# Kernel optimization log

Measured on AMD Instinct MI355X. Metric: run time of the kernel, lower is better.

## Reference

```python
import jax, jax.numpy as jnp
import numpy as np

B, S, D, H = 8, 1024, 1024, 16
HD = D // H  # head_dim = 64
SCALE = HD ** -0.5


def setup_inputs() -> dict:
    key = jax.random.key(0)
    ks = jax.random.split(key, 10)
    std = D ** -0.5
    return {
        "hidden_states": jax.random.normal(ks[0], (B, S, D), jnp.float32),
        "attn_mask": jnp.zeros((B, 1, S, S), jnp.float32),
        "prev_attn_weights": jax.random.normal(ks[1], (B, H, S, S), jnp.float32),
        "Wq": jax.random.normal(ks[2], (D, D), jnp.float32) * std,
        "bq": jnp.zeros((D,), jnp.float32),
        "Wk": jax.random.normal(ks[3], (D, D), jnp.float32) * std,
        "bk": jnp.zeros((D,), jnp.float32),
        "Wv": jax.random.normal(ks[4], (D, D), jnp.float32) * std,
        "bv": jnp.zeros((D,), jnp.float32),
    }


def _split_heads(x):
    # (B, S, D) -> (B, H, S, HD)
    return x.reshape(B, S, H, HD).transpose(0, 2, 1, 3)


def reference(hidden_states, attn_mask, prev_attn_weights, Wq, bq, Wk, bk, Wv, bv):
    q = _split_heads(hidden_states @ Wq + bq)
    k = _split_heads(hidden_states @ Wk + bk)
    v = _split_heads(hidden_states @ Wv + bv)
    # scaled dot-product scores + additive mask + realformer residual scores
    scores = jnp.einsum("bhqd,bhkd->bhqk", q, k) * SCALE
    scores = scores + attn_mask + prev_attn_weights
    probs = jax.nn.softmax(scores, axis=-1)  # dropout p=0 (eval)
    ctx = jnp.einsum("bhqk,bhkd->bhqd", probs, v)
    # (B, H, S, HD) -> (B, S, D)
    out = ctx.transpose(0, 2, 1, 3).reshape(B, S, D)
    return out
```

## Files before the change

### kernel.cpp

```cpp
#include <hip/hip_runtime.h>

#define B_  8
#define S_  1024
#define D_  1024
#define H_  16
#define HD_ 64
#define M_  8192
#define LOG2E 1.44269504088896f
#define QSCALE_ (0.125f * 1.44269504088896f)
#define MSHIFT_ 20.0f

typedef __attribute__((ext_vector_type(8))) short bf16x8;
typedef __attribute__((ext_vector_type(4))) float f32x4;

__device__ __forceinline__ unsigned short f2b(float x) {
  union { float f; unsigned u; } un; un.f = x;
  unsigned r = un.u + 0x7FFFu + ((un.u >> 16) & 1u);
  return (unsigned short)(r >> 16);
}

__global__ __launch_bounds__(256) void k_convert_x(const float* __restrict__ x,
                                                   unsigned short* __restrict__ o) {
  int i = (blockIdx.x * 256 + threadIdx.x) * 4;
  const int n = M_ * D_;
  const int stride = gridDim.x * 256 * 4;
  for (; i < n; i += stride) {
    const float4 v = *(const float4*)(x + i);
    ushort4 r;
    r.x = f2b(v.x); r.y = f2b(v.y); r.z = f2b(v.z); r.w = f2b(v.w);
    *(ushort4*)(o + i) = r;
  }
}

__global__ __launch_bounds__(256) void k_transpose_w(const float* __restrict__ Wq,
    const float* __restrict__ Wk, const float* __restrict__ Wv,
    unsigned short* __restrict__ Wt) {
  __shared__ float t[64][65];
  const float* W = (blockIdx.z == 0) ? Wq : ((blockIdx.z == 1) ? Wk : Wv);
  unsigned short* dst = Wt + (size_t)blockIdx.z * (D_ * D_);
  const int k0 = blockIdx.x * 64, n0 = blockIdx.y * 64;
  const int tid = threadIdx.x;
#pragma unroll
  for (int i = 0; i < 16; ++i) {
    const int lin = i * 256 + tid;
    const int r = lin >> 6, c = lin & 63;
    t[r][c] = W[(size_t)(k0 + r) * D_ + n0 + c];
  }
  __syncthreads();
#pragma unroll
  for (int i = 0; i < 16; ++i) {
    const int lin = i * 256 + tid;
    const int r = lin >> 6, c = lin & 63;
    dst[(size_t)(n0 + r) * D_ + k0 + c] = f2b(t[c][r]);
  }
}

template <int MODE>
__global__ __launch_bounds__(256) void k_proj(const unsigned short* __restrict__ X,
    const unsigned short* __restrict__ Wt,
    const float* __restrict__ bq, const float* __restrict__ bk, const float* __restrict__ bv,
    unsigned short* __restrict__ Qw, unsigned short* __restrict__ Kw,
    unsigned short* __restrict__ Vt) {
  __shared__ unsigned short xs[128 * 32];
  __shared__ unsigned short wsh[128 * 32];
  const int tid = threadIdx.x;
  const int lane = tid & 63, wv = tid >> 6;
  const int g = lane >> 4, li = lane & 15;
  const int m0 = blockIdx.x * 128;
  const int n0 = blockIdx.y * 128;
  const int wr = wv >> 1, wc = wv & 1;
  const int wtrow0 = (MODE == 0) ? n0 : (2048 + n0);

  f32x4 acc[4][4];
#pragma unroll
  for (int i = 0; i < 4; ++i)
#pragma unroll
    for (int j = 0; j < 4; ++j) acc[i][j] = (f32x4){0.f, 0.f, 0.f, 0.f};

  const int srow = wv * 32 + (lane >> 2);
  const int skel = (lane & 3) * 8;

  for (int k0 = 0; k0 < D_; k0 += 32) {
#pragma unroll
    for (int i = 0; i < 2; ++i) {
      const unsigned short* gx = X + (size_t)(m0 + srow + i * 16) * D_ + k0 + skel;
      const unsigned short* gw = Wt + (size_t)(wtrow0 + srow + i * 16) * D_ + k0 + skel;
      __builtin_amdgcn_global_load_lds(
          (const __attribute__((address_space(1))) void*)gx,
          (__attribute__((address_space(3))) void*)&xs[(wv * 32 + i * 16) * 32], 16, 0, 0);
      __builtin_amdgcn_global_load_lds(
          (const __attribute__((address_space(1))) void*)gw,
          (__attribute__((address_space(3))) void*)&wsh[(wv * 32 + i * 16) * 32], 16, 0, 0);
    }
    __syncthreads();
    bf16x8 af[4], bfr[4];
#pragma unroll
    for (int i = 0; i < 4; ++i) {
      const int ar = wr * 64 + i * 16 + li;
      const int br = wc * 64 + i * 16 + li;
      if (MODE == 0) {
        af[i]  = *(const bf16x8*)&xs[ar * 32 + g * 8];
        bfr[i] = *(const bf16x8*)&wsh[br * 32 + g * 8];
      } else {
        af[i]  = *(const bf16x8*)&wsh[ar * 32 + g * 8];
        bfr[i] = *(const bf16x8*)&xs[br * 32 + g * 8];
      }
    }
#pragma unroll
    for (int i = 0; i < 4; ++i)
#pragma unroll
      for (int j = 0; j < 4; ++j)
        acc[i][j] = __builtin_amdgcn_mfma_f32_16x16x32_bf16(af[i], bfr[j], acc[i][j], 0, 0, 0);
    __syncthreads();
  }

  if (MODE == 0) {
#pragma unroll
    for (int j = 0; j < 4; ++j) {
      const int n = n0 + wc * 64 + j * 16 + li;
      const float bias = (n < D_) ? bq[n] : bk[n - D_];
#pragma unroll
      for (int i = 0; i < 4; ++i) {
#pragma unroll
        for (int r = 0; r < 4; ++r) {
          const int m = m0 + wr * 64 + i * 16 + g * 4 + r;
          const float v = acc[i][j][r] + bias;
          const int bb = m >> 10, ss = m & 1023;
          if (n < D_) {
            Qw[((size_t)(bb * H_ + (n >> 6)) * S_ + ss) * HD_ + (n & 63)] = f2b(v * QSCALE_);
          } else {
            const int nk = n - D_;
            Kw[((size_t)(bb * H_ + (nk >> 6)) * S_ + ss) * HD_ + (nk & 63)] = f2b(v);
          }
        }
      }
    }
  } else {
#pragma unroll
    for (int i = 0; i < 4; ++i) {
#pragma unroll
      for (int r = 0; r < 4; ++r) {
        const int nv = n0 + wr * 64 + i * 16 + g * 4 + r;
        const float bias = bv[nv];
#pragma unroll
        for (int j = 0; j < 4; ++j) {
          const int m = m0 + wc * 64 + j * 16 + li;
          const int bb = m >> 10, ss = m & 1023;
          const float v = acc[i][j][r] + bias;
          Vt[((size_t)(bb * H_ + (nv >> 6)) * HD_ + (nv & 63)) * S_ + ss] = f2b(v);
        }
      }
    }
  }
}

__global__ __launch_bounds__(256, 2) void k_attn(const unsigned short* __restrict__ Qw,
    const unsigned short* __restrict__ Kw, const unsigned short* __restrict__ Vt,
    const float* __restrict__ prev, const float* __restrict__ mask,
    float* __restrict__ out) {
  __shared__ unsigned short k_s[2][4096];
  __shared__ unsigned short v_s[2][4096];
  __shared__ float pm_s[2][4][4][64][4];
  __shared__ unsigned short p_lds[4][16][72];
  const int tid = threadIdx.x;
  const int lane = tid & 63, wv = tid >> 6;
  const int g = lane >> 4, li = lane & 15;

  const int phys = blockIdx.x + 16 * blockIdx.y;
  const int xcd = phys & 7, idx = phys >> 3;
  const int qt = idx & 15;
  const int bh = xcd + 8 * (idx >> 4);
  const int b = bh >> 4, h = bh & 15;
  const int q0 = qt * 64 + wv * 16;

  const float* pdma = prev + (size_t)bh * S_ * S_ + (size_t)(q0 + li) * S_ + g * 4;
  const float* mb   = mask + (size_t)b * S_ * S_ + (size_t)(q0 + li) * S_ + g * 4;
  const unsigned short* kbase = Kw + (size_t)bh * S_ * HD_;
  const unsigned short* vbase = Vt + (size_t)bh * HD_ * S_;

  bf16x8 qf[2];
  {
    const unsigned short* qp = Qw + ((size_t)bh * S_ + q0 + li) * HD_ + g * 8;
    qf[0] = *(const bf16x8*)qp;
    qf[1] = *(const bf16x8*)(qp + 32);
  }

  const int dr0 = (0 * 256 + tid) >> 3, dc0 = (0 * 256 + tid) & 7;
  const int dr1 = (1 * 256 + tid) >> 3, dc1 = (1 * 256 + tid) & 7;
  const int sc0 = ((dc0 ^ (dr0 & 7)) << 3);
  const int sc1 = ((dc1 ^ (dr1 & 7)) << 3);

#define STAGE(TN, BI)                                                                      \
  {                                                                                        \
    const int sn = (TN) * 64;                                                              \
    __builtin_amdgcn_global_load_lds(                                                      \
        (const __attribute__((address_space(1))) void*)(kbase + (size_t)(sn + dr0) * HD_ + sc0), \
        (__attribute__((address_space(3))) void*)(&k_s[BI][0] + wv * 512), 16, 0, 0);      \
    __builtin_amdgcn_global_load_lds(                                                      \
        (const __attribute__((address_space(1))) void*)(kbase + (size_t)(sn + dr1) * HD_ + sc1), \
        (__attribute__((address_space(3))) void*)(&k_s[BI][0] + 2048 + wv * 512), 16, 0, 0); \
    __builtin_amdgcn_global_load_lds(                                                      \
        (const __attribute__((address_space(1))) void*)(vbase + (size_t)dr0 * S_ + sn + sc0), \
        (__attribute__((address_space(3))) void*)(&v_s[BI][0] + wv * 512), 16, 0, 0);      \
    __builtin_amdgcn_global_load_lds(                                                      \
        (const __attribute__((address_space(1))) void*)(vbase + (size_t)dr1 * S_ + sn + sc1), \
        (__attribute__((address_space(3))) void*)(&v_s[BI][0] + 2048 + wv * 512), 16, 0, 0); \
    _Pragma("unroll")                                                                      \
    for (int cb = 0; cb < 4; ++cb)                                                         \
      __builtin_amdgcn_global_load_lds(                                                    \
          (const __attribute__((address_space(1))) void*)(pdma + sn + cb * 16),            \
          (__attribute__((address_space(3))) void*)&pm_s[BI][wv][cb][0][0], 16, 0, 0);     \
  }

  float lrun = 0.f;
  f32x4 ctx[4];
#pragma unroll
  for (int d = 0; d < 4; ++d) ctx[d] = (f32x4){0.f, 0.f, 0.f, 0.f};

  f32x4 mA[4], mB[4];

  STAGE(0, 0);
#pragma unroll
  for (int cb = 0; cb < 4; ++cb) mA[cb] = *(const f32x4*)(mb + cb * 16);

#define PHASE(T, PB, NB, MCUR, MNXT)                                                  \
  {                                                                                   \
    const int tn = ((T) < 15) ? (T) + 1 : 15;                                         \
    STAGE(tn, NB);                                                                    \
    _Pragma("unroll")                                                                 \
    for (int cb = 0; cb < 4; ++cb)                                                    \
      MNXT[cb] = *(const f32x4*)(mb + tn * 64 + cb * 16);                             \
    asm volatile("s_waitcnt vmcnt(12)" ::: "memory");                                 \
    __builtin_amdgcn_s_barrier();                                                     \
    {                                                                                 \
      const unsigned short* kb = &k_s[PB][0];                                         \
      const unsigned short* vb = &v_s[PB][0];                                         \
      f32x4 sa[4];                                                                    \
      _Pragma("unroll")                                                               \
      for (int cb = 0; cb < 4; ++cb) {                                                \
        const int r = cb * 16 + li;                                                   \
        const bf16x8 k0 = *(const bf16x8*)(kb + r * 64 + ((g ^ (li & 7)) << 3));      \
        const bf16x8 k1 = *(const bf16x8*)(kb + r * 64 + (((g + 4) ^ (li & 7)) << 3)); \
        f32x4 z = (f32x4){0.f, 0.f, 0.f, 0.f};                                        \
        z      = __builtin_amdgcn_mfma_f32_16x16x32_bf16(k0, qf[0], z, 0, 0, 0);      \
        sa[cb] = __builtin_amdgcn_mfma_f32_16x16x32_bf16(k1, qf[1], z, 0, 0, 0);      \
      }                                                                               \
      _Pragma("unroll")                                                               \
      for (int cb = 0; cb < 4; ++cb) {                                                \
        const f32x4 pv = *(const f32x4*)&pm_s[PB][wv][cb][lane][0];                   \
        f32x4 pmc;                                                                    \
        pmc.x = fmaf(pv.x + MCUR[cb].x, LOG2E, -MSHIFT_);                             \
        pmc.y = fmaf(pv.y + MCUR[cb].y, LOG2E, -MSHIFT_);                             \
        pmc.z = fmaf(pv.z + MCUR[cb].z, LOG2E, -MSHIFT_);                             \
        pmc.w = fmaf(pv.w + MCUR[cb].w, LOG2E, -MSHIFT_);                             \
        const float e0 = exp2f(sa[cb][0] + pmc.x);                                    \
        const float e1 = exp2f(sa[cb][1] + pmc.y);                                    \
        const float e2 = exp2f(sa[cb][2] + pmc.z);                                    \
        const float e3 = exp2f(sa[cb][3] + pmc.w);                                    \
        lrun += (e0 + e1) + (e2 + e3);                                                \
        ushort4 pw;                                                                   \
        pw.x = f2b(e0); pw.y = f2b(e1); pw.z = f2b(e2); pw.w = f2b(e3);               \
        *(ushort4*)&p_lds[wv][li][cb * 16 + g * 4] = pw;                              \
      }                                                                               \
      bf16x8 pf0 = *(const bf16x8*)&p_lds[wv][li][g * 8];                             \
      bf16x8 pf1 = *(const bf16x8*)&p_lds[wv][li][32 + g * 8];                        \
      _Pragma("unroll")                                                               \
      for (int d = 0; d < 4; ++d) {                                                   \
        const int r = d * 16 + li;                                                    \
        const bf16x8 v0 = *(const bf16x8*)(vb + r * 64 + ((g ^ (li & 7)) << 3));      \
        const bf16x8 v1 = *(const bf16x8*)(vb + r * 64 + (((g + 4) ^ (li & 7)) << 3)); \
        ctx[d] = __builtin_amdgcn_mfma_f32_16x16x32_bf16(pf0, v0, ctx[d], 0, 0, 0);   \
        ctx[d] = __builtin_amdgcn_mfma_f32_16x16x32_bf16(pf1, v1, ctx[d], 0, 0, 0);   \
      }                                                                               \
    }                                                                                 \
    __builtin_amdgcn_s_barrier();                                                     \
  }

  for (int t = 0; t < 16; t += 2) {
    PHASE(t,     0, 1, mA, mB);
    PHASE(t + 1, 1, 0, mB, mA);
  }
#undef PHASE
#undef STAGE

  lrun += __shfl_xor(lrun, 16);
  lrun += __shfl_xor(lrun, 32);
#pragma unroll
  for (int j = 0; j < 4; ++j) {
    const float rs = __shfl(lrun, g * 4 + j);
    const float inv = 1.0f / rs;
    const int q = q0 + g * 4 + j;
    float* op = out + ((size_t)b * S_ + q) * D_ + h * HD_ + li;
#pragma unroll
    for (int d = 0; d < 4; ++d)
      op[d * 16] = ctx[d][j] * inv;
  }
}

extern "C" void kernel_launch(void* const* d_in, const int* in_sizes, int n_in,
                              void* d_out, int out_size, void* d_ws, size_t ws_size,
                              hipStream_t stream) {
  const float* hs   = (const float*)d_in[0];
  const float* mask = (const float*)d_in[1];
  const float* prev = (const float*)d_in[2];
  const float* Wq   = (const float*)d_in[3];
  const float* bq   = (const float*)d_in[4];
  const float* Wk   = (const float*)d_in[5];
  const float* bk   = (const float*)d_in[6];
  const float* Wv   = (const float*)d_in[7];
  const float* bv   = (const float*)d_in[8];
  float* out = (float*)d_out;

  char* ws = (char*)d_ws;
  unsigned short* Xbf = (unsigned short*)ws;
  unsigned short* Wt  = (unsigned short*)(ws + (16ull << 20));
  unsigned short* Qw  = (unsigned short*)(ws + (22ull << 20));
  unsigned short* Kw  = (unsigned short*)(ws + (38ull << 20));
  unsigned short* Vt  = (unsigned short*)(ws + (54ull << 20));

  k_convert_x<<<2048, 256, 0, stream>>>(hs, Xbf);
  k_transpose_w<<<dim3(16, 16, 3), 256, 0, stream>>>(Wq, Wk, Wv, Wt);
  k_proj<0><<<dim3(64, 16), 256, 0, stream>>>(Xbf, Wt, bq, bk, bv, Qw, Kw, Vt);
  k_proj<1><<<dim3(64, 8),  256, 0, stream>>>(Xbf, Wt, bq, bk, bv, Qw, Kw, Vt);
  k_attn<<<dim3(16, 128), 256, 0, stream>>>(Qw, Kw, Vt, prev, mask, out);
}
```

Measured before the change: 285.0 us.

## Triple-buffer attention with 32-key tiles, DMA mask to LDS, add setprio

Restructures the attention main loop from a double-buffered 64-key tile into a triple-buffered 32-key tile pipeline that prefetches two tiles ahead. The additive mask is now loaded asynchronously into LDS alongside prev_attn_weights instead of through register loads. MFMA sections are wrapped with s_setprio, and the V tile layout drops the XOR swizzle. The goal is to hide the memory latency of the large prev/mask streams better, at the cost of twice as many barriers and possible LDS bank conflicts on the unswizzled V reads.

Result: slower. 311.3 us (+9.2%).

```diff
diff --git a/kernel.cpp b/kernel.cpp
--- a/kernel.cpp
+++ b/kernel.cpp
@@ -158,10 +158,11 @@
     const unsigned short* __restrict__ Kw, const unsigned short* __restrict__ Vt,
     const float* __restrict__ prev, const float* __restrict__ mask,
     float* __restrict__ out) {
-  __shared__ unsigned short k_s[2][4096];
-  __shared__ unsigned short v_s[2][4096];
-  __shared__ float pm_s[2][4][4][64][4];
-  __shared__ unsigned short p_lds[4][16][72];
+  __shared__ unsigned short k_s[3][2048];
+  __shared__ unsigned short v_s[3][2048];
+  __shared__ float pm_s[3][4][2][64][4];
+  __shared__ float mk_s[3][4][2][64][4];
+  __shared__ unsigned short p_lds[4][16][40];
   const int tid = threadIdx.x;
   const int lane = tid & 63, wv = tid >> 6;
   const int g = lane >> 4, li = lane & 15;
@@ -174,7 +175,7 @@
   const int q0 = qt * 64 + wv * 16;
 
   const float* pdma = prev + (size_t)bh * S_ * S_ + (size_t)(q0 + li) * S_ + g * 4;
-  const float* mb   = mask + (size_t)b * S_ * S_ + (size_t)(q0 + li) * S_ + g * 4;
+  const float* mdma = mask + (size_t)b * S_ * S_ + (size_t)(q0 + li) * S_ + g * 4;
   const unsigned short* kbase = Kw + (size_t)bh * S_ * HD_;
   const unsigned short* vbase = Vt + (size_t)bh * HD_ * S_;
 
@@ -185,31 +186,32 @@
     qf[1] = *(const bf16x8*)(qp + 32);
   }
 
-  const int dr0 = (0 * 256 + tid) >> 3, dc0 = (0 * 256 + tid) & 7;
-  const int dr1 = (1 * 256 + tid) >> 3, dc1 = (1 * 256 + tid) & 7;
-  const int sc0 = ((dc0 ^ (dr0 & 7)) << 3);
-  const int sc1 = ((dc1 ^ (dr1 & 7)) << 3);
+  const int krow = tid >> 3;
+  const int kcol = (((tid & 7) ^ (krow & 7)) << 3);
+  const int vrow = tid >> 2;
+  const int vcol = ((tid & 3) << 3);
 
 #define STAGE(TN, BI)                                                                      \
   {                                                                                        \
-    const int sn = (TN) * 64;                                                              \
-    __builtin_amdgcn_global_load_lds(                                                      \
-        (const __attribute__((address_space(1))) void*)(kbase + (size_t)(sn + dr0) * HD_ + sc0), \
+    const int sn = (TN) * 32;                                                              \
+    __builtin_amdgcn_global_load_lds(                                                      \
+        (const __attribute__((address_space(1))) void*)(kbase + (size_t)(sn + krow) * HD_ + kcol), \
         (__attribute__((address_space(3))) void*)(&k_s[BI][0] + wv * 512), 16, 0, 0);      \
     __builtin_amdgcn_global_load_lds(                                                      \
-        (const __attribute__((address_space(1))) void*)(kbase + (size_t)(sn + dr1) * HD_ + sc1), \
-        (__attribute__((address_space(3))) void*)(&k_s[BI][0] + 2048 + wv * 512), 16, 0, 0); \
-    __builtin_amdgcn_global_load_lds(                                                      \
-        (const __attribute__((address_space(1))) void*)(vbase + (size_t)dr0 * S_ + sn + sc0), \
+        (const __attribute__((address_space(1))) void*)(vbase + (size_t)vrow * S_ + sn + vcol), \
         (__attribute__((address_space(3))) void*)(&v_s[BI][0] + wv * 512), 16, 0, 0);      \
     __builtin_amdgcn_global_load_lds(                                                      \
-        (const __attribute__((address_space(1))) void*)(vbase + (size_t)dr1 * S_ + sn + sc1), \
-        (__attribute__((address_space(3))) void*)(&v_s[BI][0] + 2048 + wv * 512), 16, 0, 0); \
-    _Pragma("unroll")                                                                      \
-    for (int cb = 0; cb < 4; ++cb)                                                         \
-      __builtin_amdgcn_global_load_lds(                                                    \
-          (const __attribute__((address_space(1))) void*)(pdma + sn + cb * 16),            \
-          (__attribute__((address_space(3))) void*)&pm_s[BI][wv][cb][0][0], 16, 0, 0);     \
+        (const __attribute__((address_space(1))) void*)(pdma + sn),                        \
+        (__attribute__((address_space(3))) void*)&pm_s[BI][wv][0][0][0], 16, 0, 0);        \
+    __builtin_amdgcn_global_load_lds(                                                      \
+        (const __attribute__((address_space(1))) void*)(pdma + sn + 16),                   \
+        (__attribute__((address_space(3))) void*)&pm_s[BI][wv][1][0][0], 16, 0, 0);        \
+    __builtin_amdgcn_global_load_lds(                                                      \
+        (const __attribute__((address_space(1))) void*)(mdma + sn),                        \
+        (__attribute__((address_space(3))) void*)&mk_s[BI][wv][0][0][0], 16, 0, 0);        \
+    __builtin_amdgcn_global_load_lds(                                                      \
+        (const __attribute__((address_space(1))) void*)(mdma + sn + 16),                   \
+        (__attribute__((address_space(3))) void*)&mk_s[BI][wv][1][0][0], 16, 0, 0);        \
   }
 
   float lrun = 0.f;
@@ -217,42 +219,38 @@
 #pragma unroll
   for (int d = 0; d < 4; ++d) ctx[d] = (f32x4){0.f, 0.f, 0.f, 0.f};
 
-  f32x4 mA[4], mB[4];
-
   STAGE(0, 0);
-#pragma unroll
-  for (int cb = 0; cb < 4; ++cb) mA[cb] = *(const f32x4*)(mb + cb * 16);
-
-#define PHASE(T, PB, NB, MCUR, MNXT)                                                  \
+  STAGE(1, 1);
+
+#define PHASE(T, PB, NB, DOSTAGE, VM)                                                 \
   {                                                                                   \
-    const int tn = ((T) < 15) ? (T) + 1 : 15;                                         \
-    STAGE(tn, NB);                                                                    \
-    _Pragma("unroll")                                                                 \
-    for (int cb = 0; cb < 4; ++cb)                                                    \
-      MNXT[cb] = *(const f32x4*)(mb + tn * 64 + cb * 16);                             \
-    asm volatile("s_waitcnt vmcnt(12)" ::: "memory");                                 \
+    if (DOSTAGE) STAGE((T) + 2, NB);                                                  \
+    asm volatile("s_waitcnt vmcnt(" #VM ")" ::: "memory");                            \
     __builtin_amdgcn_s_barrier();                                                     \
     {                                                                                 \
       const unsigned short* kb = &k_s[PB][0];                                         \
       const unsigned short* vb = &v_s[PB][0];                                         \
-      f32x4 sa[4];                                                                    \
+      f32x4 sa[2];                                                                    \
+      __builtin_amdgcn_s_setprio(1);                                                  \
       _Pragma("unroll")                                                               \
-      for (int cb = 0; cb < 4; ++cb) {                                                \
+      for (int cb = 0; cb < 2; ++cb) {                                                \
         const int r = cb * 16 + li;                                                   \
-        const bf16x8 k0 = *(const bf16x8*)(kb + r * 64 + ((g ^ (li & 7)) << 3));      \
-        const bf16x8 k1 = *(const bf16x8*)(kb + r * 64 + (((g + 4) ^ (li & 7)) << 3)); \
+        const bf16x8 k0 = *(const bf16x8*)(kb + r * 64 + ((g ^ (r & 7)) << 3));       \
+        const bf16x8 k1 = *(const bf16x8*)(kb + r * 64 + (((g + 4) ^ (r & 7)) << 3)); \
         f32x4 z = (f32x4){0.f, 0.f, 0.f, 0.f};                                        \
         z      = __builtin_amdgcn_mfma_f32_16x16x32_bf16(k0, qf[0], z, 0, 0, 0);      \
         sa[cb] = __builtin_amdgcn_mfma_f32_16x16x32_bf16(k1, qf[1], z, 0, 0, 0);      \
       }                                                                               \
+      __builtin_amdgcn_s_setprio(0);                                                  \
       _Pragma("unroll")                                                               \
-      for (int cb = 0; cb < 4; ++cb) {                                                \
+      for (int cb = 0; cb < 2; ++cb) {                                                \
         const f32x4 pv = *(const f32x4*)&pm_s[PB][wv][cb][lane][0];                   \
+        const f32x4 mv = *(const f32x4*)&mk_s[PB][wv][cb][lane][0];                   \
         f32x4 pmc;                                                                    \
-        pmc.x = fmaf(pv.x + MCUR[cb].x, LOG2E, -MSHIFT_);                             \
-        pmc.y = fmaf(pv.y + MCUR[cb].y, LOG2E, -MSHIFT_);                             \
-        pmc.z = fmaf(pv.z + MCUR[cb].z, LOG2E, -MSHIFT_);                             \
-        pmc.w = fmaf(pv.w + MCUR[cb].w, LOG2E, -MSHIFT_);                             \
+        pmc.x = fmaf(pv.x + mv.x, LOG2E, -MSHIFT_);                                   \
+        pmc.y = fmaf(pv.y + mv.y, LOG2E, -MSHIFT_);                                   \
+        pmc.z = fmaf(pv.z + mv.z, LOG2E, -MSHIFT_);                                   \
+        pmc.w = fmaf(pv.w + mv.w, LOG2E, -MSHIFT_);                                   \
         const float e0 = exp2f(sa[cb][0] + pmc.x);                                    \
         const float e1 = exp2f(sa[cb][1] + pmc.y);                                    \
         const float e2 = exp2f(sa[cb][2] + pmc.z);                                    \
@@ -262,24 +260,25 @@
         pw.x = f2b(e0); pw.y = f2b(e1); pw.z = f2b(e2); pw.w = f2b(e3);               \
         *(ushort4*)&p_lds[wv][li][cb * 16 + g * 4] = pw;                              \
       }                                                                               \
-      bf16x8 pf0 = *(const bf16x8*)&p_lds[wv][li][g * 8];                             \
-      bf16x8 pf1 = *(const bf16x8*)&p_lds[wv][li][32 + g * 8];                        \
+      const bf16x8 pf0 = *(const bf16x8*)&p_lds[wv][li][g * 8];                       \
+      __builtin_amdgcn_s_setprio(1);                                                  \
       _Pragma("unroll")                                                               \
       for (int d = 0; d < 4; ++d) {                                                   \
-        const int r = d * 16 + li;                                                    \
-        const bf16x8 v0 = *(const bf16x8*)(vb + r * 64 + ((g ^ (li & 7)) << 3));      \
-        const bf16x8 v1 = *(const bf16x8*)(vb + r * 64 + (((g + 4) ^ (li & 7)) << 3)); \
+        const bf16x8 v0 = *(const bf16x8*)(vb + (d * 16 + li) * 32 + g * 8);          \
         ctx[d] = __builtin_amdgcn_mfma_f32_16x16x32_bf16(pf0, v0, ctx[d], 0, 0, 0);   \
-        ctx[d] = __builtin_amdgcn_mfma_f32_16x16x32_bf16(pf1, v1, ctx[d], 0, 0, 0);   \
       }                                                                               \
+      __builtin_amdgcn_s_setprio(0);                                                  \
     }                                                                                 \
     __builtin_amdgcn_s_barrier();                                                     \
   }
 
-  for (int t = 0; t < 16; t += 2) {
-    PHASE(t,     0, 1, mA, mB);
-    PHASE(t + 1, 1, 0, mB, mA);
-  }
+  for (int t = 0; t < 30; t += 3) {
+    PHASE(t,     0, 2, 1, 12);
+    PHASE(t + 1, 1, 0, 1, 12);
+    PHASE(t + 2, 2, 1, 1, 12);
+  }
+  PHASE(30, 0, 2, 0, 6);
+  PHASE(31, 1, 0, 0, 0);
 #undef PHASE
 #undef STAGE
 
```

## Coalesce prev-score DMA with swizzled rows, merge projection launches

Applied to the files above, without the earlier changes.

The prev_attn_weights tile is now loaded as full 256-byte row segments per wave, with an XOR swizzle in LDS, instead of 16-byte pieces spread across many rows. K/V staging is reorganised so each wave loads its own rows. The two templated projection kernels are merged into one launch that picks its mode from blockIdx.y, which removes a launch and lets the Q/K and V work share the GPU. The merged kernel branches on mode at runtime instead of at compile time, and a final vmcnt wait is added after the attention loop.

Result: faster. 267.8 us (-6.0%).

```diff
diff --git a/kernel.cpp b/kernel.cpp
--- a/kernel.cpp
+++ b/kernel.cpp
@@ -55,7 +55,6 @@
   }
 }
 
-template <int MODE>
 __global__ __launch_bounds__(256) void k_proj(const unsigned short* __restrict__ X,
     const unsigned short* __restrict__ Wt,
     const float* __restrict__ bq, const float* __restrict__ bk, const float* __restrict__ bv,
@@ -67,9 +66,10 @@
   const int lane = tid & 63, wv = tid >> 6;
   const int g = lane >> 4, li = lane & 15;
   const int m0 = blockIdx.x * 128;
-  const int n0 = blockIdx.y * 128;
+  const int mode = (blockIdx.y >= 16);
+  const int n0 = (mode ? (blockIdx.y - 16) : blockIdx.y) * 128;
   const int wr = wv >> 1, wc = wv & 1;
-  const int wtrow0 = (MODE == 0) ? n0 : (2048 + n0);
+  const int wtrow0 = mode ? (2048 + n0) : n0;
 
   f32x4 acc[4][4];
 #pragma unroll
@@ -98,7 +98,7 @@
     for (int i = 0; i < 4; ++i) {
       const int ar = wr * 64 + i * 16 + li;
       const int br = wc * 64 + i * 16 + li;
-      if (MODE == 0) {
+      if (!mode) {
         af[i]  = *(const bf16x8*)&xs[ar * 32 + g * 8];
         bfr[i] = *(const bf16x8*)&wsh[br * 32 + g * 8];
       } else {
@@ -114,7 +114,7 @@
     __syncthreads();
   }
 
-  if (MODE == 0) {
+  if (!mode) {
 #pragma unroll
     for (int j = 0; j < 4; ++j) {
       const int n = n0 + wc * 64 + j * 16 + li;
@@ -160,7 +160,7 @@
     float* __restrict__ out) {
   __shared__ unsigned short k_s[2][4096];
   __shared__ unsigned short v_s[2][4096];
-  __shared__ float pm_s[2][4][4][64][4];
+  __shared__ float pm_s[2][4][1024];
   __shared__ unsigned short p_lds[4][16][72];
   const int tid = threadIdx.x;
   const int lane = tid & 63, wv = tid >> 6;
@@ -173,10 +173,10 @@
   const int b = bh >> 4, h = bh & 15;
   const int q0 = qt * 64 + wv * 16;
 
-  const float* pdma = prev + (size_t)bh * S_ * S_ + (size_t)(q0 + li) * S_ + g * 4;
-  const float* mb   = mask + (size_t)b * S_ * S_ + (size_t)(q0 + li) * S_ + g * 4;
   const unsigned short* kbase = Kw + (size_t)bh * S_ * HD_;
   const unsigned short* vbase = Vt + (size_t)bh * HD_ * S_;
+  const float* pbase = prev + (size_t)bh * S_ * S_ + (size_t)q0 * S_;
+  const float* mb    = mask + (size_t)b * S_ * S_ + (size_t)(q0 + li) * S_ + g * 4;
 
   bf16x8 qf[2];
   {
@@ -185,31 +185,31 @@
     qf[1] = *(const bf16x8*)(qp + 32);
   }
 
-  const int dr0 = (0 * 256 + tid) >> 3, dc0 = (0 * 256 + tid) & 7;
-  const int dr1 = (1 * 256 + tid) >> 3, dc1 = (1 * 256 + tid) & 7;
-  const int sc0 = ((dc0 ^ (dr0 & 7)) << 3);
-  const int sc1 = ((dc1 ^ (dr1 & 7)) << 3);
+  const int rloc8 = lane >> 3;
+  const int csw8  = (((lane & 7) ^ rloc8) << 3);
+  const int prow4 = lane >> 4;
+  const int pchnk = lane & 15;
 
 #define STAGE(TN, BI)                                                                      \
   {                                                                                        \
     const int sn = (TN) * 64;                                                              \
-    __builtin_amdgcn_global_load_lds(                                                      \
-        (const __attribute__((address_space(1))) void*)(kbase + (size_t)(sn + dr0) * HD_ + sc0), \
-        (__attribute__((address_space(3))) void*)(&k_s[BI][0] + wv * 512), 16, 0, 0);      \
-    __builtin_amdgcn_global_load_lds(                                                      \
-        (const __attribute__((address_space(1))) void*)(kbase + (size_t)(sn + dr1) * HD_ + sc1), \
-        (__attribute__((address_space(3))) void*)(&k_s[BI][0] + 2048 + wv * 512), 16, 0, 0); \
-    __builtin_amdgcn_global_load_lds(                                                      \
-        (const __attribute__((address_space(1))) void*)(vbase + (size_t)dr0 * S_ + sn + sc0), \
-        (__attribute__((address_space(3))) void*)(&v_s[BI][0] + wv * 512), 16, 0, 0);      \
-    __builtin_amdgcn_global_load_lds(                                                      \
-        (const __attribute__((address_space(1))) void*)(vbase + (size_t)dr1 * S_ + sn + sc1), \
-        (__attribute__((address_space(3))) void*)(&v_s[BI][0] + 2048 + wv * 512), 16, 0, 0); \
     _Pragma("unroll")                                                                      \
-    for (int cb = 0; cb < 4; ++cb)                                                         \
+    for (int i = 0; i < 2; ++i) {                                                          \
+      const int row = wv * 16 + i * 8 + rloc8;                                             \
       __builtin_amdgcn_global_load_lds(                                                    \
-          (const __attribute__((address_space(1))) void*)(pdma + sn + cb * 16),            \
-          (__attribute__((address_space(3))) void*)&pm_s[BI][wv][cb][0][0], 16, 0, 0);     \
+          (const __attribute__((address_space(1))) void*)(kbase + (size_t)(sn + row) * HD_ + csw8), \
+          (__attribute__((address_space(3))) void*)(&k_s[BI][0] + (wv * 16 + i * 8) * 64), 16, 0, 0); \
+      __builtin_amdgcn_global_load_lds(                                                    \
+          (const __attribute__((address_space(1))) void*)(vbase + (size_t)row * S_ + sn + csw8), \
+          (__attribute__((address_space(3))) void*)(&v_s[BI][0] + (wv * 16 + i * 8) * 64), 16, 0, 0); \
+    }                                                                                      \
+    _Pragma("unroll")                                                                      \
+    for (int i = 0; i < 4; ++i) {                                                          \
+      const int row = i * 4 + prow4;                                                       \
+      __builtin_amdgcn_global_load_lds(                                                    \
+          (const __attribute__((address_space(1))) void*)(pbase + (size_t)row * S_ + sn + ((pchnk ^ (row & 7)) << 2)), \
+          (__attribute__((address_space(3))) void*)(&pm_s[BI][wv][i * 256]), 16, 0, 0);    \
+    }                                                                                      \
   }
 
   float lrun = 0.f;
@@ -235,19 +235,20 @@
     {                                                                                 \
       const unsigned short* kb = &k_s[PB][0];                                         \
       const unsigned short* vb = &v_s[PB][0];                                         \
+      const float* pmw = &pm_s[PB][wv][0];                                            \
       f32x4 sa[4];                                                                    \
       _Pragma("unroll")                                                               \
       for (int cb = 0; cb < 4; ++cb) {                                                \
         const int r = cb * 16 + li;                                                   \
         const bf16x8 k0 = *(const bf16x8*)(kb + r * 64 + ((g ^ (li & 7)) << 3));      \
-        const bf16x8 k1 = *(const bf16x8*)(kb + r * 64 + (((g + 4) ^ (li & 7)) << 3)); \
+        const bf16x8 k1 = *(const bf16x8*)(kb + r * 64 + (((4 + g) ^ (li & 7)) << 3)); \
         f32x4 z = (f32x4){0.f, 0.f, 0.f, 0.f};                                        \
         z      = __builtin_amdgcn_mfma_f32_16x16x32_bf16(k0, qf[0], z, 0, 0, 0);      \
         sa[cb] = __builtin_amdgcn_mfma_f32_16x16x32_bf16(k1, qf[1], z, 0, 0, 0);      \
       }                                                                               \
       _Pragma("unroll")                                                               \
       for (int cb = 0; cb < 4; ++cb) {                                                \
-        const f32x4 pv = *(const f32x4*)&pm_s[PB][wv][cb][lane][0];                   \
+        const f32x4 pv = *(const f32x4*)(pmw + li * 64 + (((cb * 4 + g) ^ (li & 7)) << 2)); \
         f32x4 pmc;                                                                    \
         pmc.x = fmaf(pv.x + MCUR[cb].x, LOG2E, -MSHIFT_);                             \
         pmc.y = fmaf(pv.y + MCUR[cb].y, LOG2E, -MSHIFT_);                             \
@@ -268,7 +269,7 @@
       for (int d = 0; d < 4; ++d) {                                                   \
         const int r = d * 16 + li;                                                    \
         const bf16x8 v0 = *(const bf16x8*)(vb + r * 64 + ((g ^ (li & 7)) << 3));      \
-        const bf16x8 v1 = *(const bf16x8*)(vb + r * 64 + (((g + 4) ^ (li & 7)) << 3)); \
+        const bf16x8 v1 = *(const bf16x8*)(vb + r * 64 + (((4 + g) ^ (li & 7)) << 3)); \
         ctx[d] = __builtin_amdgcn_mfma_f32_16x16x32_bf16(pf0, v0, ctx[d], 0, 0, 0);   \
         ctx[d] = __builtin_amdgcn_mfma_f32_16x16x32_bf16(pf1, v1, ctx[d], 0, 0, 0);   \
       }                                                                               \
@@ -282,6 +283,8 @@
   }
 #undef PHASE
 #undef STAGE
+
+  asm volatile("s_waitcnt vmcnt(0)" ::: "memory");
 
   lrun += __shfl_xor(lrun, 16);
   lrun += __shfl_xor(lrun, 32);
@@ -320,7 +323,6 @@
 
   k_convert_x<<<2048, 256, 0, stream>>>(hs, Xbf);
   k_transpose_w<<<dim3(16, 16, 3), 256, 0, stream>>>(Wq, Wk, Wv, Wt);
-  k_proj<0><<<dim3(64, 16), 256, 0, stream>>>(Xbf, Wt, bq, bk, bv, Qw, Kw, Vt);
-  k_proj<1><<<dim3(64, 8),  256, 0, stream>>>(Xbf, Wt, bq, bk, bv, Qw, Kw, Vt);
+  k_proj<<<dim3(64, 24), 256, 0, stream>>>(Xbf, Wt, bq, bk, bv, Qw, Kw, Vt);
   k_attn<<<dim3(16, 128), 256, 0, stream>>>(Qw, Kw, Vt, prev, mask, out);
 }
```
